# Performance work log

Hardware: AMD Instinct MI355X
Metric: run time of the kernel (lower is better)

## Reference

```python
import jax, jax.numpy as jnp
import numpy as np

B, S, D_IN = 2, 2048, 2048
D_OUT, H, RD, L = 2048, 16, 64, 512
HD = D_OUT // H  # 128
ROPE_BASE = 10000.0
EPS = 1e-6


def _rmsnorm(x, w):
    # RMSNorm over last dim
    ms = jnp.mean(jnp.square(x), axis=-1, keepdims=True)
    return x * jax.lax.rsqrt(ms + EPS) * w


def _apply_rope(x, offset):
    # x: [B, H, T, RD]; GPT-NeoX style rotary embedding
    T, rd = x.shape[-2], x.shape[-1]
    pos = (offset + jnp.arange(T)).astype(jnp.float32)  # [T]
    inv_freq = 1.0 / (ROPE_BASE ** (jnp.arange(0, rd, 2, dtype=jnp.float32) / rd))  # [rd/2]
    ang = pos[:, None] * inv_freq[None, :]              # [T, rd/2]
    cos = jnp.cos(jnp.concatenate([ang, ang], axis=-1))  # [T, rd]
    sin = jnp.sin(jnp.concatenate([ang, ang], axis=-1))
    x1, x2 = jnp.split(x, 2, axis=-1)
    rot = jnp.concatenate([-x2, x1], axis=-1)
    return x * cos + rot * sin


def setup_inputs() -> dict:
    key = jax.random.key(0)
    ks = jax.random.split(key, 8)
    sc = 0.02
    return {
        "x": jax.random.normal(ks[0], (B, S, D_IN), jnp.float32),
        "W_DKV": jax.random.normal(ks[1], (L, D_IN), jnp.float32) * sc,
        "W_KRope": jax.random.normal(ks[2], (H * RD, D_IN), jnp.float32) * sc,
        "W_Q": jax.random.normal(ks[3], (D_OUT + H * RD, D_IN), jnp.float32) * sc,
        "W_UK": jax.random.normal(ks[4], (D_OUT, L), jnp.float32) * sc,
        "W_UV": jax.random.normal(ks[5], (D_OUT, L), jnp.float32) * sc,
        "W_O": jax.random.normal(ks[6], (D_IN, D_OUT), jnp.float32) * sc,
        "kv_norm_w": jnp.ones((L,), jnp.float32),
        "offset": 0,
    }


def reference(x, W_DKV, W_KRope, W_Q, W_UK, W_UV, W_O, kv_norm_w, offset):
    b, s, _ = x.shape
    # compressed latent KV (shared across heads)
    c_kv = _rmsnorm(x @ W_DKV.T, kv_norm_w)                      # [B,S,L]
    k_rope = (x @ W_KRope.T).reshape(b, s, H, RD).transpose(0, 2, 1, 3)  # [B,H,S,RD]
    # eval path: fused query projection
    q_total = x @ W_Q.T                                          # [B,S,D_OUT+H*RD]
    q_content = q_total[..., :D_OUT].reshape(b, s, H, HD).transpose(0, 2, 1, 3)  # [B,H,S,HD]
    q_rope = q_total[..., D_OUT:].reshape(b, s, H, RD).transpose(0, 2, 1, 3)     # [B,H,S,RD]
    q_rope = _apply_rope(q_rope, offset)
    k_rope = _apply_rope(k_rope, offset)
    # absorb W_UK into query: q_abs[b,h,s,l]
    w_uk = W_UK.reshape(H, HD, L)
    q_abs = jnp.einsum('bhsd,hdl->bhsl', q_content, w_uk)
    # attention scores against the shared latent + per-head rope keys
    scores = (jnp.einsum('bhsl,btl->bhst', q_abs, c_kv)
              + jnp.einsum('bhsr,bhtr->bhst', q_rope, k_rope))
    scores = scores * jax.lax.rsqrt(jnp.float32(HD + RD))
    t = c_kv.shape[1]
    causal = jnp.arange(t)[None, :] > (jnp.arange(s)[:, None] + offset)  # [S,T]
    scores = jnp.where(causal[None, None], -jnp.inf, scores)
    attn = jax.nn.softmax(scores, axis=-1)                       # [B,H,S,T]
    # attend in latent space, then absorb W_UV on the way out
    ctx_lat = jnp.einsum('bhst,btl->bhsl', attn, c_kv)           # [B,H,S,L]
    w_uv = W_UV.reshape(H, HD, L)
    ctx = jnp.einsum('bhsl,hdl->bhsd', ctx_lat, w_uv)            # [B,H,S,HD]
    ctx = ctx.transpose(0, 2, 1, 3).reshape(b, s, D_OUT)
    return ctx @ W_O.T
```

## Files before the change

kernel.cpp:

```cpp
#include <hip/hip_runtime.h>
#include <hip/hip_bf16.h>
#include <math.h>

#define B_    2
#define S_    2048
#define DIN   2048
#define DOUT  2048
#define H_    16
#define RD_   64
#define L_    512
#define HD_   128
#define BS_   (B_*S_)

typedef __attribute__((ext_vector_type(8))) short bf16x8;
typedef __attribute__((ext_vector_type(4))) float f32x4;

__device__ __forceinline__ short f2bs(float f) {
    __hip_bfloat16 h = __float2bfloat16(f);
    return *reinterpret_cast<short*>(&h);
}
__device__ __forceinline__ float bs2f(short s) {
    unsigned u = ((unsigned)(unsigned short)s) << 16;
    return __uint_as_float(u);
}

__device__ __forceinline__ void gld16(const void* g, void* l) {
    __builtin_amdgcn_global_load_lds(
        (const __attribute__((address_space(1))) unsigned int*)g,
        (__attribute__((address_space(3))) unsigned int*)l, 16, 0, 0);
}

__global__ __launch_bounds__(256) void cast_bf(const float* __restrict__ in,
                                               short* __restrict__ out, int n8)
{
    int i = blockIdx.x * 256 + threadIdx.x;
    if (i >= n8) return;
    float4 a = ((const float4*)in)[i*2], b = ((const float4*)in)[i*2+1];
    bf16x8 t;
    t[0]=f2bs(a.x); t[1]=f2bs(a.y); t[2]=f2bs(a.z); t[3]=f2bs(a.w);
    t[4]=f2bs(b.x); t[5]=f2bs(b.y); t[6]=f2bs(b.z); t[7]=f2bs(b.w);
    ((bf16x8*)out)[i] = t;
}

__global__ __launch_bounds__(256, 4) void gemm_bf(
    const short* __restrict__ A, const short* __restrict__ Bw,
    float* __restrict__ Cf, short* __restrict__ Cb, int N, int K)
{
    __shared__ short As[128*40];
    __shared__ short Bs[128*40];
    const int tid = threadIdx.x;
    const int m0 = blockIdx.y << 7, n0 = blockIdx.x << 7;
    const int w = tid >> 6, lane = tid & 63;
    const int quad = lane >> 4, n16 = lane & 15;
    const int mw = (w & 1) << 6, nw = (w >> 1) << 6;

    f32x4 acc[4][4];
    #pragma unroll
    for (int mt = 0; mt < 4; mt++)
        #pragma unroll
        for (int nt = 0; nt < 4; nt++) acc[mt][nt] = (f32x4){0.f,0.f,0.f,0.f};

    for (int k0 = 0; k0 < K; k0 += 32) {
        #pragma unroll
        for (int i = 0; i < 2; i++) {
            int c = i*256 + tid;
            int m = c >> 2, kc = c & 3;
            *(bf16x8*)(As + m*40 + kc*8) =
                *(const bf16x8*)(A + (long long)(m0 + m)*K + k0 + kc*8);
            *(bf16x8*)(Bs + m*40 + kc*8) =
                *(const bf16x8*)(Bw + (long long)(n0 + m)*K + k0 + kc*8);
        }
        __syncthreads();
        bf16x8 af[4], bfr[4];
        #pragma unroll
        for (int t = 0; t < 4; t++) {
            af[t]  = *(const bf16x8*)(As + (mw + t*16 + n16)*40 + quad*8);
            bfr[t] = *(const bf16x8*)(Bs + (nw + t*16 + n16)*40 + quad*8);
        }
        #pragma unroll
        for (int mt = 0; mt < 4; mt++)
            #pragma unroll
            for (int nt = 0; nt < 4; nt++)
                acc[mt][nt] = __builtin_amdgcn_mfma_f32_16x16x32_bf16(
                                  af[mt], bfr[nt], acc[mt][nt], 0, 0, 0);
        __syncthreads();
    }

    #pragma unroll
    for (int mt = 0; mt < 4; mt++)
        #pragma unroll
        for (int nt = 0; nt < 4; nt++)
            #pragma unroll
            for (int r = 0; r < 4; r++) {
                long long row = m0 + mw + mt*16 + quad*4 + r;
                int col = n0 + nw + nt*16 + n16;
                if (Cf) Cf[row*(long long)N + col] = acc[mt][nt][r];
                else    Cb[row*(long long)N + col] = f2bs(acc[mt][nt][r]);
            }
}

__global__ __launch_bounds__(256) void rmsnorm_bf(const float* __restrict__ ckv,
                                                  const float* __restrict__ w,
                                                  short* __restrict__ out)
{
    const int row = blockIdx.x;
    const int tid = threadIdx.x;
    const float* p = ckv + (long long)row * L_;
    float v0 = p[tid], v1 = p[tid + 256];
    float ss = v0 * v0 + v1 * v1;
    #pragma unroll
    for (int o = 32; o >= 1; o >>= 1) ss += __shfl_xor(ss, o);
    __shared__ float wsum[4];
    if ((tid & 63) == 0) wsum[tid >> 6] = ss;
    __syncthreads();
    float tot = wsum[0] + wsum[1] + wsum[2] + wsum[3];
    float scale = rsqrtf(tot * (1.0f / (float)L_) + 1e-6f);
    out[(long long)row * L_ + tid]       = f2bs(v0 * scale * w[tid]);
    out[(long long)row * L_ + tid + 256] = f2bs(v1 * scale * w[tid + 256]);
}

__global__ __launch_bounds__(256) void vup_transpose(const short* __restrict__ in,
                                                     short* __restrict__ out)
{
    __shared__ short tile[64][72];
    const int b = blockIdx.z, t0 = blockIdx.x * 64, c0 = blockIdx.y * 64;
    const int tid = threadIdx.x;
    #pragma unroll
    for (int i = 0; i < 16; i++) {
        int idx = i*256 + tid, r = idx >> 6, c = idx & 63;
        tile[r][c] = in[((long long)(b*S_ + t0 + r))*2048 + c0 + c];
    }
    __syncthreads();
    #pragma unroll
    for (int i = 0; i < 16; i++) {
        int idx = i*256 + tid, r = idx >> 6, c = idx & 63;
        out[((long long)(b*S_ + c0 + r))*2048 + t0 + c] = tile[c][r];
    }
}

__global__ __launch_bounds__(256) void rope_kernel(short* __restrict__ q_bf,
                                                   short* __restrict__ kr_bf,
                                                   const int* __restrict__ offp)
{
    const int offset = offp[0];
    long long idx = (long long)blockIdx.x * 256 + threadIdx.x;
    int r = (int)(idx & 31);
    long long t = idx >> 5;
    int h = (int)(t % H_);
    long long m = t / H_;
    int s = (int)(m % S_);

    float inv = (float)exp(-9.210340371976184 * ((double)r / 32.0));
    float ang = (float)(offset + s) * inv;
    float sn, cs;
    sincosf(ang, &sn, &cs);

    short* q = q_bf + m * 3072 + DOUT + h * RD_;
    float x1 = bs2f(q[r]), x2 = bs2f(q[r + 32]);
    q[r]      = f2bs(x1 * cs - x2 * sn);
    q[r + 32] = f2bs(x2 * cs + x1 * sn);

    short* kk = kr_bf + m * (H_ * RD_) + h * RD_;
    x1 = bs2f(kk[r]); x2 = bs2f(kk[r + 32]);
    kk[r]      = f2bs(x1 * cs - x2 * sn);
    kk[r + 32] = f2bs(x2 * cs + x1 * sn);
}

#define TKC0 0
#define TKR0 16384
#define TVT0 24576
#define TPP0 40960

__global__ __launch_bounds__(512)
__attribute__((amdgpu_waves_per_eu(2, 2)))
void flash_mha(
    const short* __restrict__ q_bf,
    const short* __restrict__ K_up,
    const short* __restrict__ kr_bf,
    const short* __restrict__ V_upT,
    const int* __restrict__ offp,
    short* __restrict__ ctx_bf)
{
    __shared__ short lds[50176];
    const int offset = offp[0];
    const int bh = blockIdx.y;
    const int b = bh >> 4, h = bh & 15;
    const int r0 = (int)(gridDim.x - 1 - blockIdx.x) * 128;
    const int tid = threadIdx.x;
    const int w = tid >> 6, lane = tid & 63;
    const int quad = lane >> 4, n16 = lane & 15;
    const int rx3 = (n16 & 7) << 3;
    const float scale = rsqrtf((float)(HD_ + RD_));

    const int l4 = lane >> 4, g16 = lane & 15;
    const int l8 = lane >> 3, g8 = lane & 7;

    const short* kc_src = K_up  + ((long long)b*S_)*2048 + h*HD_;
    const short* kr_src = kr_bf + ((long long)b*S_)*1024 + h*RD_;
    const short* vt_src = V_upT + ((long long)(b*S_ + h*HD_))*2048;

    auto stage = [&](int tk, int bf) {
        #pragma unroll
        for (int j = 0; j < 2; j++) {
            int r4 = (w*2 + j)*4;
            int row = r4 + l4;
            int gs = g16 ^ (row & 7);
            gld16(kc_src + (long long)(tk + row)*2048 + gs*8,
                  (void*)(lds + TKC0 + bf*8192 + r4*128));
        }
        {
            int row = w*8 + l8;
            int gs = g8 ^ (l8 & 7);
            gld16(kr_src + (long long)(tk + row)*1024 + gs*8,
                  (void*)(lds + TKR0 + bf*4096 + w*512));
        }
        #pragma unroll
        for (int j = 0; j < 2; j++) {
            int d8 = (w*2 + j)*8;
            int d = d8 + l8;
            int gs = g8 ^ (l8 & 7);
            gld16(vt_src + (long long)d*2048 + tk + gs*8,
                  (void*)(lds + TVT0 + bf*8192 + d8*64));
        }
    };

    stage(0, 0);

    bf16x8 qf[6];
    {
        const short* qp = q_bf + ((long long)(b*S_ + r0 + w*16 + n16))*3072;
        #pragma unroll
        for (int ks = 0; ks < 4; ks++)
            qf[ks] = *(const bf16x8*)(qp + h*HD_ + ks*32 + quad*8);
        #pragma unroll
        for (int ks = 0; ks < 2; ks++)
            qf[4+ks] = *(const bf16x8*)(qp + DOUT + h*RD_ + ks*32 + quad*8);
    }

    f32x4 Oacc[8];
    #pragma unroll
    for (int v = 0; v < 8; v++) Oacc[v] = (f32x4){0.f,0.f,0.f,0.f};
    float mrun[4] = {-INFINITY,-INFINITY,-INFINITY,-INFINITY};
    float lrun[4] = {0.f,0.f,0.f,0.f};

    int tmax = r0 + 128 + offset;
    if (tmax > S_) tmax = S_;

    for (int t0 = 0, bf = 0; t0 < tmax; t0 += 64, bf ^= 1) {
        asm volatile("s_waitcnt vmcnt(0)" ::: "memory");
        __builtin_amdgcn_s_barrier();
        __builtin_amdgcn_sched_barrier(0);

        if (t0 + 64 < tmax) stage(t0 + 64, bf ^ 1);

        const short* kcb = lds + TKC0 + bf*8192;
        const short* krb = lds + TKR0 + bf*4096;
        f32x4 Sf[4];
        #pragma unroll
        for (int nt = 0; nt < 4; nt++) {
            f32x4 a = {0.f,0.f,0.f,0.f};
            const short* kc = kcb + (nt*16 + n16)*128;
            #pragma unroll
            for (int ks = 0; ks < 4; ks++)
                a = __builtin_amdgcn_mfma_f32_16x16x32_bf16(
                        qf[ks], *(const bf16x8*)(kc + ((ks*32 + quad*8) ^ rx3)),
                        a, 0, 0, 0);
            const short* kr = krb + (nt*16 + n16)*64;
            a = __builtin_amdgcn_mfma_f32_16x16x32_bf16(
                    qf[4], *(const bf16x8*)(kr + ((quad*8) ^ rx3)), a, 0, 0, 0);
            a = __builtin_amdgcn_mfma_f32_16x16x32_bf16(
                    qf[5], *(const bf16x8*)(kr + ((32 + quad*8) ^ rx3)), a, 0, 0, 0);
            Sf[nt] = a;
        }

        float al[4];
        bool need = false;
        #pragma unroll
        for (int r = 0; r < 4; r++) {
            const int srow = r0 + w*16 + quad*4 + r;
            float e0[4]; float tm = -INFINITY;
            #pragma unroll
            for (int nt = 0; nt < 4; nt++) {
                int t = t0 + nt*16 + n16;
                float s = (t <= srow + offset) ? Sf[nt][r]*scale : -INFINITY;
                e0[nt] = s; tm = fmaxf(tm, s);
            }
            tm = fmaxf(tm, __shfl_xor(tm, 1));
            tm = fmaxf(tm, __shfl_xor(tm, 2));
            tm = fmaxf(tm, __shfl_xor(tm, 4));
            tm = fmaxf(tm, __shfl_xor(tm, 8));
            if (tm > mrun[r] + 8.f) {
                al[r] = __expf(mrun[r] - tm);
                mrun[r] = tm;
                need = true;
            } else al[r] = 1.f;
            float ps = 0.f;
            #pragma unroll
            for (int nt = 0; nt < 4; nt++) {
                float ex = __expf(e0[nt] - mrun[r]);
                ps += ex;
                lds[TPP0 + w*1152 + (quad*4 + r)*72 + nt*16 + n16] = f2bs(ex);
            }
            ps += __shfl_xor(ps, 1);
            ps += __shfl_xor(ps, 2);
            ps += __shfl_xor(ps, 4);
            ps += __shfl_xor(ps, 8);
            lrun[r] = lrun[r]*al[r] + ps;
        }
        if (__any((int)need)) {
            #pragma unroll
            for (int v = 0; v < 8; v++) {
                Oacc[v][0] *= al[0]; Oacc[v][1] *= al[1];
                Oacc[v][2] *= al[2]; Oacc[v][3] *= al[3];
            }
        }

        const short* vtb = lds + TVT0 + bf*8192;
        bf16x8 pf0 = *(const bf16x8*)(lds + TPP0 + w*1152 + n16*72 + quad*8);
        bf16x8 pf1 = *(const bf16x8*)(lds + TPP0 + w*1152 + n16*72 + 32 + quad*8);
        const int vo0 = (quad*8) ^ rx3, vo1 = (32 + quad*8) ^ rx3;
        #pragma unroll
        for (int v = 0; v < 8; v++) {
            const short* vb = vtb + (v*16 + n16)*64;
            Oacc[v] = __builtin_amdgcn_mfma_f32_16x16x32_bf16(
                          pf0, *(const bf16x8*)(vb + vo0), Oacc[v], 0, 0, 0);
            Oacc[v] = __builtin_amdgcn_mfma_f32_16x16x32_bf16(
                          pf1, *(const bf16x8*)(vb + vo1), Oacc[v], 0, 0, 0);
        }
    }

    float inv[4];
    #pragma unroll
    for (int r = 0; r < 4; r++) inv[r] = 1.0f / lrun[r];
    #pragma unroll
    for (int v = 0; v < 8; v++)
        #pragma unroll
        for (int r = 0; r < 4; r++) {
            long long row = (long long)b*S_ + r0 + w*16 + quad*4 + r;
            ctx_bf[row*2048 + h*HD_ + v*16 + n16] = f2bs(Oacc[v][r]*inv[r]);
        }
}

extern "C" void kernel_launch(void* const* d_in, const int* in_sizes, int n_in,
                              void* d_out, int out_size, void* d_ws, size_t ws_size,
                              hipStream_t stream)
{
    const float* x       = (const float*)d_in[0];
    const float* W_DKV   = (const float*)d_in[1];
    const float* W_KRope = (const float*)d_in[2];
    const float* W_Q     = (const float*)d_in[3];
    const float* W_UK    = (const float*)d_in[4];
    const float* W_UV    = (const float*)d_in[5];
    const float* W_O     = (const float*)d_in[6];
    const float* kvnw    = (const float*)d_in[7];
    const int*   offp    = (const int*)d_in[8];
    float* out = (float*)d_out;

    float* ws = (float*)d_ws;
    float* c_kv    = ws;
    short* x_bf    = (short*)(c_kv + 2097152);
    short* q_bf    = x_bf    + 8388608;
    short* kr_bf   = q_bf    + 12582912;
    short* c_kv_bf = kr_bf   + 4194304;
    short* wuk_bf  = c_kv_bf + 2097152;
    short* wuv_bf  = wuk_bf  + 1048576;
    short* wdkv_bf = wuv_bf  + 1048576;
    short* wkr_bf  = wdkv_bf + 1048576;
    short* wq_bf   = wkr_bf  + 2097152;
    short* wo_bf   = wq_bf   + 6291456;
    short* ctx_bf  = wo_bf   + 4194304;
    short* V_upT   = ctx_bf  + 8388608;
    short* K_up    = x_bf;
    short* V_up    = ctx_bf;

    dim3 blk(256);

    cast_bf<<<4096, blk, 0, stream>>>(x, x_bf, 1048576);
    cast_bf<<<512,  blk, 0, stream>>>(W_DKV, wdkv_bf, 131072);
    cast_bf<<<1024, blk, 0, stream>>>(W_KRope, wkr_bf, 262144);
    cast_bf<<<3072, blk, 0, stream>>>(W_Q, wq_bf, 786432);
    cast_bf<<<2048, blk, 0, stream>>>(W_O, wo_bf, 524288);
    cast_bf<<<512,  blk, 0, stream>>>(W_UK, wuk_bf, 131072);
    cast_bf<<<512,  blk, 0, stream>>>(W_UV, wuv_bf, 131072);

    gemm_bf<<<dim3(3072/128, 32), blk, 0, stream>>>(
        x_bf, wq_bf, nullptr, q_bf, 3072, 2048);
    gemm_bf<<<dim3(1024/128, 32), blk, 0, stream>>>(
        x_bf, wkr_bf, nullptr, kr_bf, 1024, 2048);
    gemm_bf<<<dim3(512/128, 32), blk, 0, stream>>>(
        x_bf, wdkv_bf, c_kv, nullptr, 512, 2048);
    rmsnorm_bf<<<4096, blk, 0, stream>>>(c_kv, kvnw, c_kv_bf);

    gemm_bf<<<dim3(2048/128, 32), blk, 0, stream>>>(
        c_kv_bf, wuk_bf, nullptr, K_up, 2048, 512);
    gemm_bf<<<dim3(2048/128, 32), blk, 0, stream>>>(
        c_kv_bf, wuv_bf, nullptr, V_up, 2048, 512);
    vup_transpose<<<dim3(32, 32, 2), blk, 0, stream>>>(V_up, V_upT);

    rope_kernel<<<8192, blk, 0, stream>>>(q_bf, kr_bf, offp);

    flash_mha<<<dim3(S_/128, B_*H_), dim3(512), 0, stream>>>(
        q_bf, K_up, kr_bf, V_upT, offp, ctx_bf);

    gemm_bf<<<dim3(2048/128, 32), blk, 0, stream>>>(
        ctx_bf, wo_bf, out, nullptr, 2048, 2048);
}
```

Baseline: 582.8 us.

## Use direct-to-LDS swizzled GEMM loads, compute V transposed, lazy softmax rescale

```diff
diff --git a/kernel.cpp b/kernel.cpp
--- a/kernel.cpp
+++ b/kernel.cpp
@@ -46,13 +46,15 @@
     const short* __restrict__ A, const short* __restrict__ Bw,
     float* __restrict__ Cf, short* __restrict__ Cb, int N, int K)
 {
-    __shared__ short As[128*40];
-    __shared__ short Bs[128*40];
+    __shared__ short As[128*32];
+    __shared__ short Bs[128*32];
     const int tid = threadIdx.x;
     const int m0 = blockIdx.y << 7, n0 = blockIdx.x << 7;
     const int w = tid >> 6, lane = tid & 63;
     const int quad = lane >> 4, n16 = lane & 15;
     const int mw = (w & 1) << 6, nw = (w >> 1) << 6;
+    const int lr = lane >> 2, cg = lane & 3;
+    const int swr = (quad ^ (n16 & 3)) << 3;
 
     f32x4 acc[4][4];
     #pragma unroll
@@ -62,20 +64,19 @@
 
     for (int k0 = 0; k0 < K; k0 += 32) {
         #pragma unroll
-        for (int i = 0; i < 2; i++) {
-            int c = i*256 + tid;
-            int m = c >> 2, kc = c & 3;
-            *(bf16x8*)(As + m*40 + kc*8) =
-                *(const bf16x8*)(A + (long long)(m0 + m)*K + k0 + kc*8);
-            *(bf16x8*)(Bs + m*40 + kc*8) =
-                *(const bf16x8*)(Bw + (long long)(n0 + m)*K + k0 + kc*8);
+        for (int jj = 0; jj < 2; jj++) {
+            int rb = (jj*4 + w)*16;
+            int r = rb + lr;
+            int sc = (cg ^ (r & 3)) << 3;
+            gld16(A  + (long long)(m0 + r)*K + k0 + sc, (void*)(As + rb*32));
+            gld16(Bw + (long long)(n0 + r)*K + k0 + sc, (void*)(Bs + rb*32));
         }
         __syncthreads();
         bf16x8 af[4], bfr[4];
         #pragma unroll
         for (int t = 0; t < 4; t++) {
-            af[t]  = *(const bf16x8*)(As + (mw + t*16 + n16)*40 + quad*8);
-            bfr[t] = *(const bf16x8*)(Bs + (nw + t*16 + n16)*40 + quad*8);
+            af[t]  = *(const bf16x8*)(As + (mw + t*16 + n16)*32 + swr);
+            bfr[t] = *(const bf16x8*)(Bs + (nw + t*16 + n16)*32 + swr);
         }
         #pragma unroll
         for (int mt = 0; mt < 4; mt++)
@@ -117,25 +118,6 @@
     float scale = rsqrtf(tot * (1.0f / (float)L_) + 1e-6f);
     out[(long long)row * L_ + tid]       = f2bs(v0 * scale * w[tid]);
     out[(long long)row * L_ + tid + 256] = f2bs(v1 * scale * w[tid + 256]);
-}
-
-__global__ __launch_bounds__(256) void vup_transpose(const short* __restrict__ in,
-                                                     short* __restrict__ out)
-{
-    __shared__ short tile[64][72];
-    const int b = blockIdx.z, t0 = blockIdx.x * 64, c0 = blockIdx.y * 64;
-    const int tid = threadIdx.x;
-    #pragma unroll
-    for (int i = 0; i < 16; i++) {
-        int idx = i*256 + tid, r = idx >> 6, c = idx & 63;
-        tile[r][c] = in[((long long)(b*S_ + t0 + r))*2048 + c0 + c];
-    }
-    __syncthreads();
-    #pragma unroll
-    for (int i = 0; i < 16; i++) {
-        int idx = i*256 + tid, r = idx >> 6, c = idx & 63;
-        out[((long long)(b*S_ + c0 + r))*2048 + t0 + c] = tile[c][r];
-    }
 }
 
 __global__ __launch_bounds__(256) void rope_kernel(short* __restrict__ q_bf,
@@ -273,46 +255,51 @@
             Sf[nt] = a;
         }
 
-        float al[4];
-        bool need = false;
+        float e0[4][4], lm[4];
         #pragma unroll
         for (int r = 0; r < 4; r++) {
             const int srow = r0 + w*16 + quad*4 + r;
-            float e0[4]; float tm = -INFINITY;
+            lm[r] = -INFINITY;
             #pragma unroll
             for (int nt = 0; nt < 4; nt++) {
                 int t = t0 + nt*16 + n16;
                 float s = (t <= srow + offset) ? Sf[nt][r]*scale : -INFINITY;
-                e0[nt] = s; tm = fmaxf(tm, s);
+                e0[r][nt] = s;
+                lm[r] = fmaxf(lm[r], s);
             }
-            tm = fmaxf(tm, __shfl_xor(tm, 1));
-            tm = fmaxf(tm, __shfl_xor(tm, 2));
-            tm = fmaxf(tm, __shfl_xor(tm, 4));
-            tm = fmaxf(tm, __shfl_xor(tm, 8));
-            if (tm > mrun[r] + 8.f) {
-                al[r] = __expf(mrun[r] - tm);
-                mrun[r] = tm;
-                need = true;
-            } else al[r] = 1.f;
-            float ps = 0.f;
-            #pragma unroll
-            for (int nt = 0; nt < 4; nt++) {
-                float ex = __expf(e0[nt] - mrun[r]);
-                ps += ex;
-                lds[TPP0 + w*1152 + (quad*4 + r)*72 + nt*16 + n16] = f2bs(ex);
+        }
+        bool trig = (lm[0] > mrun[0] + 8.f) | (lm[1] > mrun[1] + 8.f)
+                  | (lm[2] > mrun[2] + 8.f) | (lm[3] > mrun[3] + 8.f);
+        if (__any((int)trig)) {
+            float al[4];
+            #pragma unroll
+            for (int r = 0; r < 4; r++) {
+                float tm = lm[r];
+                tm = fmaxf(tm, __shfl_xor(tm, 1));
+                tm = fmaxf(tm, __shfl_xor(tm, 2));
+                tm = fmaxf(tm, __shfl_xor(tm, 4));
+                tm = fmaxf(tm, __shfl_xor(tm, 8));
+                if (tm > mrun[r]) { al[r] = __expf(mrun[r] - tm); mrun[r] = tm; }
+                else al[r] = 1.f;
             }
-            ps += __shfl_xor(ps, 1);
-            ps += __shfl_xor(ps, 2);
-            ps += __shfl_xor(ps, 4);
-            ps += __shfl_xor(ps, 8);
-            lrun[r] = lrun[r]*al[r] + ps;
-        }
-        if (__any((int)need)) {
             #pragma unroll
             for (int v = 0; v < 8; v++) {
                 Oacc[v][0] *= al[0]; Oacc[v][1] *= al[1];
                 Oacc[v][2] *= al[2]; Oacc[v][3] *= al[3];
             }
+            lrun[0] *= al[0]; lrun[1] *= al[1];
+            lrun[2] *= al[2]; lrun[3] *= al[3];
+        }
+        #pragma unroll
+        for (int r = 0; r < 4; r++) {
+            float ps = 0.f;
+            #pragma unroll
+            for (int nt = 0; nt < 4; nt++) {
+                float ex = __expf(e0[r][nt] - mrun[r]);
+                ps += ex;
+                lds[TPP0 + w*1152 + (quad*4 + r)*72 + nt*16 + n16] = f2bs(ex);
+            }
+            lrun[r] += ps;
         }
 
         const short* vtb = lds + TVT0 + bf*8192;
@@ -331,7 +318,14 @@
 
     float inv[4];
     #pragma unroll
-    for (int r = 0; r < 4; r++) inv[r] = 1.0f / lrun[r];
+    for (int r = 0; r < 4; r++) {
+        float s = lrun[r];
+        s += __shfl_xor(s, 1);
+        s += __shfl_xor(s, 2);
+        s += __shfl_xor(s, 4);
+        s += __shfl_xor(s, 8);
+        inv[r] = 1.0f / s;
+    }
     #pragma unroll
     for (int v = 0; v < 8; v++)
         #pragma unroll
@@ -371,7 +365,6 @@
     short* ctx_bf  = wo_bf   + 4194304;
     short* V_upT   = ctx_bf  + 8388608;
     short* K_up    = x_bf;
-    short* V_up    = ctx_bf;
 
     dim3 blk(256);
 
@@ -393,9 +386,11 @@
 
     gemm_bf<<<dim3(2048/128, 32), blk, 0, stream>>>(
         c_kv_bf, wuk_bf, nullptr, K_up, 2048, 512);
-    gemm_bf<<<dim3(2048/128, 32), blk, 0, stream>>>(
-        c_kv_bf, wuv_bf, nullptr, V_up, 2048, 512);
-    vup_transpose<<<dim3(32, 32, 2), blk, 0, stream>>>(V_up, V_upT);
+    gemm_bf<<<dim3(2048/128, 16), blk, 0, stream>>>(
+        wuv_bf, c_kv_bf, nullptr, V_upT, 2048, 512);
+    gemm_bf<<<dim3(2048/128, 16), blk, 0, stream>>>(
+        wuv_bf, c_kv_bf + (long long)S_*512, nullptr,
+        V_upT + (long long)S_*2048, 2048, 512);
 
     rope_kernel<<<8192, blk, 0, stream>>>(q_bf, kr_bf, offp);
 
```

New measurement: 528.5 us. -9.3%, faster.
